# Kernel optimization log

Hardware: AMD Instinct MI355X
Metric: run time of the kernel (lower is better)

Reference implementation:

```python
import jax, jax.numpy as jnp
import numpy as np

THRESH = 1.0
SLOPE = 25.0  # fast_sigmoid surrogate slope
B, T, C_IN = 64, 512, 32
HID, TS, K = 128, 4, 3
C_OUT = HID * TS

@jax.custom_vjp
def spike_fn(x):
    # Heaviside forward, fast-sigmoid surrogate backward (matches snntorch surrogate.fast_sigmoid(slope=25))
    return (x > 0).astype(x.dtype)

def _spike_fwd(x):
    return spike_fn(x), x

def _spike_bwd(x, g):
    return (g / (SLOPE * jnp.abs(x) + 1.0) ** 2,)

spike_fn.defvjp(_spike_fwd, _spike_bwd)


def setup_inputs() -> dict:
    key = jax.random.key(0)
    ks = jax.random.split(key, 4)
    return {
        "x": jax.random.normal(ks[0], (B, T, C_IN), jnp.float32),
        "conv_w": jax.random.normal(ks[1], (C_OUT, C_IN, K), jnp.float32) / np.sqrt(C_IN * K).astype(np.float32),
        "conv_b": jax.random.normal(ks[2], (C_OUT,), jnp.float32) * 0.01,
        "bn_gamma": jnp.ones((C_OUT,), jnp.float32),
        "bn_beta": jnp.zeros((C_OUT,), jnp.float32),
        "bn_mean": jax.random.normal(ks[3], (C_OUT,), jnp.float32) * 0.1,
        "bn_var": jnp.ones((C_OUT,), jnp.float32),
        "lif_beta": jnp.full((HID,), 0.9, jnp.float32),
    }


def reference(x, conv_w, conv_b, bn_gamma, bn_beta, bn_mean, bn_var, lif_beta):
    # Conv1d(input -> hidden*Ts, k=3, pad=1): x (B,T,C) -> NCH layout
    h = jax.lax.conv_general_dilated(
        x.transpose(0, 2, 1), conv_w, (1,), [(K // 2, K // 2)],
        dimension_numbers=("NCH", "OIH", "NCH"))  # (B, C_OUT, T)
    h = h + conv_b[None, :, None]
    # BatchNorm1d in eval mode (running stats)
    scale = bn_gamma * jax.lax.rsqrt(bn_var + 1e-5)
    h = (h - bn_mean[None, :, None]) * scale[None, :, None] + bn_beta[None, :, None]
    # (B, C_OUT, T) -> (B, T, Ts, HID) -> (Ts*T, B, HID) time-major spike input
    h = h.transpose(0, 2, 1).reshape(B, T * TS, HID).transpose(1, 0, 2)

    beta = jnp.clip(lif_beta, 0.0, 1.0)

    def step(mem, h_t):
        # snntorch Leaky (reset_mechanism='subtract'): reset from previous mem, detached
        reset = jax.lax.stop_gradient((mem > THRESH).astype(mem.dtype))
        mem = beta * mem + h_t - reset * THRESH
        spk = spike_fn(mem - THRESH)
        return mem, (spk, mem)

    mem0 = jnp.zeros((B, HID), x.dtype)
    _, (spk_rec, mem_rec) = jax.lax.scan(step, mem0, h)
    return spk_rec, mem_rec  # each (Ts*T, B, HID)
```

## Files before the change

kernel.cpp:

```cpp
#include <hip/hip_runtime.h>

#define T_LEN 512
#define CIN   32
#define HIDN  128
#define TSUB  4
#define NB    64
#define TT    64
#define NT2   2048
#define COLS  8192
#define CHUNK 32
#define NCHUNK (NT2 / CHUNK)

__global__ __launch_bounds__(256) void conv_bn_kernel(
    const float* __restrict__ x,
    const float* __restrict__ w,
    const float* __restrict__ cb,
    const float* __restrict__ gam,
    const float* __restrict__ bet,
    const float* __restrict__ mean,
    const float* __restrict__ var,
    float* __restrict__ h)
{
    __shared__ float xs[66 * 36];
    __shared__ float ws[128 * 100];
    __shared__ float scs[128];
    __shared__ float bbs[128];

    const int t0  = blockIdx.x * TT;
    const int s   = blockIdx.y;
    const int b   = blockIdx.z;
    const int tid = threadIdx.x;

    for (int idx = tid; idx < 66 * 32; idx += 256) {
        int r = idx >> 5, ci = idx & 31;
        int t = t0 + r - 1;
        xs[r * 36 + ci] = (t >= 0 && t < T_LEN) ? x[(b * T_LEN + t) * CIN + ci] : 0.0f;
    }
    for (int idx = tid; idx < 128 * 96; idx += 256) {
        int row = idx / 96, j = idx - row * 96;
        int k = j >> 5, i = j & 31;
        ws[row * 100 + j] = w[(s * HIDN + row) * (CIN * 3) + i * 3 + k];
    }
    if (tid < 128) {
        int c = s * HIDN + tid;
        float sc = gam[c] * rsqrtf(var[c] + 1e-5f);
        scs[tid] = sc;
        bbs[tid] = (cb[c] - mean[c]) * sc + bet[c];
    }
    __syncthreads();

    const int tc = tid & 31;
    const int tt = tid >> 5;

    float acc[4][8];
#pragma unroll
    for (int a = 0; a < 4; ++a)
#pragma unroll
        for (int q = 0; q < 8; ++q) acc[a][q] = 0.0f;

    for (int j0 = 0; j0 < 96; j0 += 4) {
        const int k  = j0 >> 5;
        const int i0 = j0 & 31;
        float4 wv[4];
#pragma unroll
        for (int cc = 0; cc < 4; ++cc)
            wv[cc] = *reinterpret_cast<const float4*>(&ws[(tc + cc * 32) * 100 + j0]);
#pragma unroll
        for (int tq = 0; tq < 8; ++tq) {
            float4 xv = *reinterpret_cast<const float4*>(&xs[(tt * 8 + tq + k) * 36 + i0]);
#pragma unroll
            for (int cc = 0; cc < 4; ++cc) {
                acc[cc][tq] = fmaf(wv[cc].x, xv.x, acc[cc][tq]);
                acc[cc][tq] = fmaf(wv[cc].y, xv.y, acc[cc][tq]);
                acc[cc][tq] = fmaf(wv[cc].z, xv.z, acc[cc][tq]);
                acc[cc][tq] = fmaf(wv[cc].w, xv.w, acc[cc][tq]);
            }
        }
    }

#pragma unroll
    for (int cc = 0; cc < 4; ++cc) {
        const int hid = tc + cc * 32;
        const float sc = scs[hid], bb = bbs[hid];
#pragma unroll
        for (int tq = 0; tq < 8; ++tq) {
            const int t = t0 + tt * 8 + tq;
            h[((t * TSUB + s) * NB + b) * HIDN + hid] = fmaf(acc[cc][tq], sc, bb);
        }
    }
}

__global__ __launch_bounds__(64) void lif_pass1_kernel(
    const float* __restrict__ h,
    const float* __restrict__ lifb,
    float* __restrict__ out)
{
    const int col = blockIdx.x * 64 + threadIdx.x;
    const int hid = col & (HIDN - 1);
    float beta = lifb[hid];
    beta = fminf(fmaxf(beta, 0.0f), 1.0f);

    float* __restrict__ memo = out + (size_t)NT2 * COLS;

    float mem = 0.0f;
    constexpr int PF = 64;
    float hv[PF];
#pragma unroll
    for (int i = 0; i < PF; ++i) hv[i] = h[i * COLS + col];

    for (int t0 = 0; t0 < NT2; t0 += PF) {
        float hn[PF];
        if (t0 + PF < NT2) {
#pragma unroll
            for (int i = 0; i < PF; ++i) hn[i] = h[(t0 + PF + i) * COLS + col];
        }
#pragma unroll
        for (int i = 0; i < PF; ++i) {
            const float reset = (mem > 1.0f) ? 1.0f : 0.0f;
            mem = __fsub_rn(__fadd_rn(__fmul_rn(beta, mem), hv[i]), reset);
            if ((i & (CHUNK - 1)) == CHUNK - 1) {
                const int t = t0 + i;
                if (t < NT2 - 1) memo[t * COLS + col] = mem;
            }
        }
#pragma unroll
        for (int i = 0; i < PF; ++i) hv[i] = hn[i];
    }
}

__global__ __launch_bounds__(256) void lif_pass2_kernel(
    const float* __restrict__ h,
    const float* __restrict__ lifb,
    float* __restrict__ out)
{
    const int chunk = blockIdx.y;
    const int col   = blockIdx.x * 256 + threadIdx.x;
    const int hid   = col & (HIDN - 1);
    float beta = lifb[hid];
    beta = fminf(fmaxf(beta, 0.0f), 1.0f);

    float* __restrict__ spk  = out;
    float* __restrict__ memo = out + (size_t)NT2 * COLS;

    const int tbase = chunk * CHUNK;
    float mem = (chunk == 0) ? 0.0f : memo[(tbase - 1) * COLS + col];

    constexpr int PF = 16;
    float hv[PF];
#pragma unroll
    for (int i = 0; i < PF; ++i) hv[i] = h[(tbase + i) * COLS + col];

    for (int tt = 0; tt < CHUNK; tt += PF) {
        float hn[PF];
        if (tt + PF < CHUNK) {
#pragma unroll
            for (int i = 0; i < PF; ++i) hn[i] = h[(tbase + tt + PF + i) * COLS + col];
        }
#pragma unroll
        for (int i = 0; i < PF; ++i) {
            const float reset = (mem > 1.0f) ? 1.0f : 0.0f;
            mem = __fsub_rn(__fadd_rn(__fmul_rn(beta, mem), hv[i]), reset);
            const int idx = (tbase + tt + i) * COLS + col;
            spk[idx]  = (mem > 1.0f) ? 1.0f : 0.0f;
            memo[idx] = mem;
        }
#pragma unroll
        for (int i = 0; i < PF; ++i) hv[i] = hn[i];
    }
}

extern "C" void kernel_launch(void* const* d_in, const int* in_sizes, int n_in,
                              void* d_out, int out_size, void* d_ws, size_t ws_size,
                              hipStream_t stream) {
    const float* x    = (const float*)d_in[0];
    const float* w    = (const float*)d_in[1];
    const float* cb   = (const float*)d_in[2];
    const float* gam  = (const float*)d_in[3];
    const float* bet  = (const float*)d_in[4];
    const float* mean = (const float*)d_in[5];
    const float* var  = (const float*)d_in[6];
    const float* lifb = (const float*)d_in[7];

    float* h = (float*)d_ws;

    dim3 gA(T_LEN / TT, TSUB, NB);
    conv_bn_kernel<<<gA, 256, 0, stream>>>(x, w, cb, gam, bet, mean, var, h);

    lif_pass1_kernel<<<COLS / 64, 64, 0, stream>>>(h, lifb, (float*)d_out);

    dim3 gC(COLS / 256, NCHUNK);
    lif_pass2_kernel<<<gC, 256, 0, stream>>>(h, lifb, (float*)d_out);
}
```

Baseline: 288.1 us.

## Transpose conv output to time-contiguous layout for vectorized LIF loads

The intermediate conv/BN buffer changes from time-major [t][s][b][hid] to a [s][col][t] layout. Each LIF thread can then fetch its time series with float4 loads instead of one scalar load per time step, and the conv epilogue writes float4 pairs along time. The cost is that neighbouring lanes now sit a full time row apart (2 KB stride). That makes both the conv stores and the LIF loads uncoalesced across a wavefront and relies on cache to reuse partially-fetched lines.

```diff
diff --git a/kernel.cpp b/kernel.cpp
--- a/kernel.cpp
+++ b/kernel.cpp
@@ -11,6 +11,8 @@
 #define CHUNK 32
 #define NCHUNK (NT2 / CHUNK)
 
+#define HT_IDX(s, col, t) ((((size_t)(s) * COLS + (size_t)(col)) * T_LEN) + (size_t)(t))
+
 __global__ __launch_bounds__(256) void conv_bn_kernel(
     const float* __restrict__ x,
     const float* __restrict__ w,
@@ -19,7 +21,7 @@
     const float* __restrict__ bet,
     const float* __restrict__ mean,
     const float* __restrict__ var,
-    float* __restrict__ h)
+    float* __restrict__ hT)
 {
     __shared__ float xs[66 * 36];
     __shared__ float ws[128 * 100];
@@ -82,90 +84,104 @@
     for (int cc = 0; cc < 4; ++cc) {
         const int hid = tc + cc * 32;
         const float sc = scs[hid], bb = bbs[hid];
-#pragma unroll
-        for (int tq = 0; tq < 8; ++tq) {
-            const int t = t0 + tt * 8 + tq;
-            h[((t * TSUB + s) * NB + b) * HIDN + hid] = fmaf(acc[cc][tq], sc, bb);
-        }
+        float4 v0, v1;
+        v0.x = fmaf(acc[cc][0], sc, bb);
+        v0.y = fmaf(acc[cc][1], sc, bb);
+        v0.z = fmaf(acc[cc][2], sc, bb);
+        v0.w = fmaf(acc[cc][3], sc, bb);
+        v1.x = fmaf(acc[cc][4], sc, bb);
+        v1.y = fmaf(acc[cc][5], sc, bb);
+        v1.z = fmaf(acc[cc][6], sc, bb);
+        v1.w = fmaf(acc[cc][7], sc, bb);
+        float* dst = hT + HT_IDX(s, b * HIDN + hid, t0 + tt * 8);
+        *reinterpret_cast<float4*>(dst)     = v0;
+        *reinterpret_cast<float4*>(dst + 4) = v1;
     }
 }
 
 __global__ __launch_bounds__(64) void lif_pass1_kernel(
-    const float* __restrict__ h,
+    const float* __restrict__ hT,
     const float* __restrict__ lifb,
     float* __restrict__ out)
 {
     const int col = blockIdx.x * 64 + threadIdx.x;
     const int hid = col & (HIDN - 1);
-    float beta = lifb[hid];
-    beta = fminf(fmaxf(beta, 0.0f), 1.0f);
+    float beta = fminf(fmaxf(lifb[hid], 0.0f), 1.0f);
 
     float* __restrict__ memo = out + (size_t)NT2 * COLS;
 
+    const float4* p[4];
+#pragma unroll
+    for (int s = 0; s < 4; ++s)
+        p[s] = reinterpret_cast<const float4*>(hT + HT_IDX(s, col, 0));
+
+    float4 hq[4][4];
+#pragma unroll
+    for (int bq = 0; bq < 4; ++bq)
+#pragma unroll
+        for (int s = 0; s < 4; ++s) hq[bq][s] = p[s][bq];
+
     float mem = 0.0f;
-    constexpr int PF = 64;
-    float hv[PF];
-#pragma unroll
-    for (int i = 0; i < PF; ++i) hv[i] = h[i * COLS + col];
-
-    for (int t0 = 0; t0 < NT2; t0 += PF) {
-        float hn[PF];
-        if (t0 + PF < NT2) {
-#pragma unroll
-            for (int i = 0; i < PF; ++i) hn[i] = h[(t0 + PF + i) * COLS + col];
-        }
-#pragma unroll
-        for (int i = 0; i < PF; ++i) {
-            const float reset = (mem > 1.0f) ? 1.0f : 0.0f;
-            mem = __fsub_rn(__fadd_rn(__fmul_rn(beta, mem), hv[i]), reset);
-            if ((i & (CHUNK - 1)) == CHUNK - 1) {
-                const int t = t0 + i;
-                if (t < NT2 - 1) memo[t * COLS + col] = mem;
+
+    for (int m0 = 0; m0 < 128; m0 += 4) {
+#pragma unroll
+        for (int bq = 0; bq < 4; ++bq) {
+            const int m = m0 + bq;
+            const float* hb = reinterpret_cast<const float*>(&hq[bq][0]);
+#pragma unroll
+            for (int j = 0; j < 16; ++j) {
+                const float hval = hb[(j & 3) * 4 + (j >> 2)];
+                const float reset = (mem > 1.0f) ? 1.0f : 0.0f;
+                mem = __fsub_rn(__fadd_rn(__fmul_rn(beta, mem), hval), reset);
+                if (j == 15 && (bq & 1) == 1) {
+                    const int tp = m * 16 + 15;
+                    if (tp < NT2 - 1)
+                        memo[(size_t)tp * COLS + col] = mem;
+                }
+            }
+            if (m + 4 < 128) {
+#pragma unroll
+                for (int s = 0; s < 4; ++s) hq[bq][s] = p[s][m + 4];
             }
         }
-#pragma unroll
-        for (int i = 0; i < PF; ++i) hv[i] = hn[i];
     }
 }
 
 __global__ __launch_bounds__(256) void lif_pass2_kernel(
-    const float* __restrict__ h,
+    const float* __restrict__ hT,
     const float* __restrict__ lifb,
     float* __restrict__ out)
 {
     const int chunk = blockIdx.y;
     const int col   = blockIdx.x * 256 + threadIdx.x;
     const int hid   = col & (HIDN - 1);
-    float beta = lifb[hid];
-    beta = fminf(fmaxf(beta, 0.0f), 1.0f);
+    float beta = fminf(fmaxf(lifb[hid], 0.0f), 1.0f);
 
     float* __restrict__ spk  = out;
     float* __restrict__ memo = out + (size_t)NT2 * COLS;
 
-    const int tbase = chunk * CHUNK;
-    float mem = (chunk == 0) ? 0.0f : memo[(tbase - 1) * COLS + col];
-
-    constexpr int PF = 16;
-    float hv[PF];
-#pragma unroll
-    for (int i = 0; i < PF; ++i) hv[i] = h[(tbase + i) * COLS + col];
-
-    for (int tt = 0; tt < CHUNK; tt += PF) {
-        float hn[PF];
-        if (tt + PF < CHUNK) {
-#pragma unroll
-            for (int i = 0; i < PF; ++i) hn[i] = h[(tbase + tt + PF + i) * COLS + col];
-        }
-#pragma unroll
-        for (int i = 0; i < PF; ++i) {
-            const float reset = (mem > 1.0f) ? 1.0f : 0.0f;
-            mem = __fsub_rn(__fadd_rn(__fmul_rn(beta, mem), hv[i]), reset);
-            const int idx = (tbase + tt + i) * COLS + col;
-            spk[idx]  = (mem > 1.0f) ? 1.0f : 0.0f;
-            memo[idx] = mem;
-        }
-#pragma unroll
-        for (int i = 0; i < PF; ++i) hv[i] = hn[i];
+    const int tpb = chunk * CHUNK;
+    const int tb  = tpb >> 2;
+
+    float4 hq[4][2];
+#pragma unroll
+    for (int s = 0; s < 4; ++s) {
+        const float4* ps = reinterpret_cast<const float4*>(hT + HT_IDX(s, col, tb));
+        hq[s][0] = ps[0];
+        hq[s][1] = ps[1];
+    }
+
+    float mem = (chunk == 0) ? 0.0f : memo[(size_t)(tpb - 1) * COLS + col];
+
+#pragma unroll
+    for (int j = 0; j < 32; ++j) {
+        const float* hb = reinterpret_cast<const float*>(&hq[j & 3][0]);
+        const float hval = hb[j >> 2];
+        const float reset = (mem > 1.0f) ? 1.0f : 0.0f;
+        mem = __fsub_rn(__fadd_rn(__fmul_rn(beta, mem), hval), reset);
+        const size_t idx = (size_t)(tpb + j) * COLS + col;
+        spk[idx]  = (mem > 1.0f) ? 1.0f : 0.0f;
+        memo[idx] = mem;
     }
 }
 
@@ -181,13 +197,13 @@
     const float* var  = (const float*)d_in[6];
     const float* lifb = (const float*)d_in[7];
 
-    float* h = (float*)d_ws;
+    float* hT = (float*)d_ws;
 
     dim3 gA(T_LEN / TT, TSUB, NB);
-    conv_bn_kernel<<<gA, 256, 0, stream>>>(x, w, cb, gam, bet, mean, var, h);
-
-    lif_pass1_kernel<<<COLS / 64, 64, 0, stream>>>(h, lifb, (float*)d_out);
+    conv_bn_kernel<<<gA, 256, 0, stream>>>(x, w, cb, gam, bet, mean, var, hT);
+
+    lif_pass1_kernel<<<COLS / 64, 64, 0, stream>>>(hT, lifb, (float*)d_out);
 
     dim3 gC(COLS / 256, NCHUNK);
-    lif_pass2_kernel<<<gC, 256, 0, stream>>>(h, lifb, (float*)d_out);
-}
+    lif_pass2_kernel<<<gC, 256, 0, stream>>>(hT, lifb, (float*)d_out);
+}
```

New measurement: 268.3 us. 1.07x faster.
